# Optimization experiments

Hardware: AMD Instinct MI355X
Metric: run time of the kernel (lower is better)

The kernel has to match this reference:

```python
import jax, jax.numpy as jnp
import numpy as np

NUM_RELATIONS = 8
N_NODES = 50000
N_EDGES = 640000
D_IN = 128
D_HID = 128
N_CLASSES = 16


def rgcn_layer(x, edge_index, edge_type, edge_weight, W):
    # Faithful to ExtendedRGCNConv.forward: per-relation propagate with
    # message = (edge_weight * x_j) @ W[rel]  (== edge_weight * (x_j @ W[rel]))
    # aggregated by scatter-MEAN (PyG RGCNConv default aggr), summed over relations.
    # No root weight / bias (the override skips them).
    src, dst = edge_index[0], edge_index[1]
    num_nodes = x.shape[0]
    out = jnp.zeros((num_nodes, W.shape[2]), dtype=x.dtype)
    for r in range(W.shape[0]):
        sel = edge_type == r
        w = jnp.where(sel, edge_weight, jnp.zeros((), x.dtype))  # [E]
        h = x @ W[r]                                             # [N, out]
        msg = h[src] * w[:, None]                                # [E, out]
        s = jax.ops.segment_sum(msg, dst, num_segments=num_nodes)
        cnt = jax.ops.segment_sum(sel.astype(x.dtype), dst, num_segments=num_nodes)
        out = out + s / jnp.maximum(cnt, 1.0)[:, None]
    return out


def setup_inputs() -> dict:
    key = jax.random.key(0)
    k1, k2, k3, k4, k5, k6 = jax.random.split(key, 6)
    x = jax.random.normal(k1, (N_NODES, D_IN), dtype=jnp.float32)
    edge_index = jax.random.randint(k2, (2, N_EDGES), 0, N_NODES, dtype=jnp.int64)
    edge_type = jax.random.randint(k3, (N_EDGES,), 0, NUM_RELATIONS, dtype=jnp.int64)
    edge_attr = jax.random.uniform(k4, (N_EDGES,), dtype=jnp.float32)
    # Xavier-uniform-ish relation weight banks
    b1 = (6.0 / (D_IN + D_HID)) ** 0.5
    W1 = jax.random.uniform(k5, (NUM_RELATIONS, D_IN, D_HID), minval=-b1, maxval=b1, dtype=jnp.float32)
    b2 = (6.0 / (D_HID + N_CLASSES)) ** 0.5
    W2 = jax.random.uniform(k6, (NUM_RELATIONS, D_HID, N_CLASSES), minval=-b2, maxval=b2, dtype=jnp.float32)
    return {"x": x, "edge_index": edge_index, "edge_type": edge_type, "edge_attr": edge_attr, "W1": W1, "W2": W2}


def reference(x, edge_index, edge_type, edge_attr, W1, W2):
    h = rgcn_layer(x, edge_index, edge_type, edge_attr, W1)
    h = jax.nn.relu(h)
    h = rgcn_layer(h, edge_index, edge_type, edge_attr, W2)
    return jax.nn.log_softmax(h, axis=1)
```

## Files before the change

### kernel.cpp

```cpp
#include <hip/hip_runtime.h>
#include <hip/hip_bf16.h>
#include <math.h>

#define NN 50000
#define EE 640000
#define DD 128
#define NREL 8
#define NCLS 16
#define NBUCK (NREL * NN)
#define SCAN_NB ((NBUCK + 255) / 256)
#define NBIN 64
#define RECCAP 40

typedef __attribute__((ext_vector_type(8))) short short8;
typedef __attribute__((ext_vector_type(4))) float f32x4;

__device__ __forceinline__ float bflo(unsigned u) { return __uint_as_float(u << 16); }
__device__ __forceinline__ float bfhi(unsigned u) { return __uint_as_float(u & 0xffff0000u); }
__device__ __forceinline__ float bf2f(ushort u) { return __uint_as_float(((unsigned)u) << 16); }
__device__ __forceinline__ ushort f2b(float f) {
  unsigned u = __float_as_uint(f);
  u += 0x7fff + ((u >> 16) & 1);
  return (ushort)(u >> 16);
}


__global__ __launch_bounds__(256) void count_kernel(const int* __restrict__ ei,
                                                    const int* __restrict__ et,
                                                    int* __restrict__ cnt) {
  int t = blockIdx.x * 256 + threadIdx.x;
  if (t < EE) {
    int key = ei[EE + t] * NREL + et[t];
    atomicAdd(&cnt[key], 1);
  }
}

__global__ __launch_bounds__(256) void scan1_kernel(const int* __restrict__ cnt,
                                                    int* __restrict__ off,
                                                    int* __restrict__ bsum) {
  __shared__ int s[256];
  const int tid = threadIdx.x;
  const int i = blockIdx.x * 256 + tid;
  int v = (i < NBUCK) ? cnt[i] : 0;
  s[tid] = v;
  __syncthreads();
#pragma unroll
  for (int o = 1; o < 256; o <<= 1) {
    int t2 = (tid >= o) ? s[tid - o] : 0;
    __syncthreads();
    s[tid] += t2;
    __syncthreads();
  }
  if (i < NBUCK) off[i] = s[tid] - v;
  if (tid == 255) bsum[blockIdx.x] = s[255];
}

__global__ __launch_bounds__(256) void scan2_kernel(const int* __restrict__ bsum,
                                                    int* __restrict__ bpre) {
  __shared__ int s[256];
  __shared__ int carry;
  const int tid = threadIdx.x;
  if (tid == 0) carry = 0;
  __syncthreads();
  const int chunks = (SCAN_NB + 255) / 256;
  for (int c = 0; c < chunks; c++) {
    int idx = c * 256 + tid;
    int v = (idx < SCAN_NB) ? bsum[idx] : 0;
    s[tid] = v;
    __syncthreads();
#pragma unroll
    for (int o = 1; o < 256; o <<= 1) {
      int t2 = (tid >= o) ? s[tid - o] : 0;
      __syncthreads();
      s[tid] += t2;
      __syncthreads();
    }
    if (idx < SCAN_NB) bpre[idx] = carry + s[tid] - v;
    __syncthreads();
    if (tid == 255) carry += s[255];
    __syncthreads();
  }
}

__global__ __launch_bounds__(256) void scan3_kernel(int* __restrict__ off,
                                                    const int* __restrict__ bpre,
                                                    int* __restrict__ cursor,
                                                    int* __restrict__ hist) {
  int i = blockIdx.x * 256 + threadIdx.x;
  if (i < NBUCK) {
    int o = off[i] + bpre[i >> 8];
    off[i] = o;
    cursor[i] = o;
  }
  if (i < NBIN) hist[i] = 0;
  if (i == 0) off[NBUCK] = EE;
}

__global__ __launch_bounds__(256) void bucket_kernel(const int* __restrict__ ei,
                                                     const int* __restrict__ et,
                                                     const float* __restrict__ ew,
                                                     const int* __restrict__ cnt,
                                                     int* __restrict__ cursor,
                                                     uint2* __restrict__ rec) {
  int e = blockIdx.x * 256 + threadIdx.x;
  if (e >= EE) return;
  int r = et[e];
  int key = ei[EE + e] * NREL + r;
  float scale = ew[e] / fmaxf((float)cnt[key], 1.0f);
  int pos = atomicAdd(&cursor[key], 1);
  rec[pos] = make_uint2((unsigned)ei[e] | ((unsigned)r << 16), __float_as_uint(scale));
}


__global__ __launch_bounds__(256) void vhist_kernel(const int* __restrict__ off,
                                                    int* __restrict__ hist) {
  __shared__ int lh[NBIN];
  const int tid = threadIdx.x;
  if (tid < NBIN) lh[tid] = 0;
  __syncthreads();
  int v = blockIdx.x * 256 + tid;
  if (v < NN) {
    int deg = off[v * NREL + NREL] - off[v * NREL];
    atomicAdd(&lh[min(deg, NBIN - 1)], 1);
  }
  __syncthreads();
  if (tid < NBIN && lh[tid] > 0) atomicAdd(&hist[tid], lh[tid]);
}

__global__ __launch_bounds__(256) void scan64_kernel(const int* __restrict__ hist,
                                                     int* __restrict__ binCur) {
  __shared__ int s[NBIN];
  const int tid = threadIdx.x;
  if (tid < NBIN) s[tid] = hist[tid];
  __syncthreads();
#pragma unroll
  for (int o = 1; o < NBIN; o <<= 1) {
    int t2 = (tid < NBIN && tid >= o) ? s[tid - o] : 0;
    __syncthreads();
    if (tid < NBIN) s[tid] += t2;
    __syncthreads();
  }
  if (tid < NBIN) binCur[tid] = s[tid] - hist[tid];
}

__global__ __launch_bounds__(256) void vqbuild_kernel(const int* __restrict__ off,
                                                      int* __restrict__ binCur,
                                                      int* __restrict__ vqueue) {
  __shared__ int lh[NBIN];
  __shared__ int lbase[NBIN];
  const int tid = threadIdx.x;
  const int v = blockIdx.x * 256 + tid;
  int bin = -1, lpos = 0;
  if (tid < NBIN) lh[tid] = 0;
  __syncthreads();
  if (v < NN) {
    int deg = off[v * NREL + NREL] - off[v * NREL];
    bin = min(deg, NBIN - 1);
    lpos = atomicAdd(&lh[bin], 1);
  }
  __syncthreads();
  if (tid < NBIN && lh[tid] > 0) lbase[tid] = atomicAdd(&binCur[tid], lh[tid]);
  __syncthreads();
  if (bin >= 0) vqueue[lbase[bin] + lpos] = v;
}

#define XQ (NN * DD / 4)
__global__ __launch_bounds__(256) void pack_kernel(const float* __restrict__ x,
                                                   const float* __restrict__ W1,
                                                   const float* __restrict__ W2,
                                                   ushort* __restrict__ xb,
                                                   ushort* __restrict__ W1Tc,
                                                   ushort* __restrict__ W2T) {
  int t = blockIdx.x * 256 + threadIdx.x;
  if (t < XQ) {
    float4 v = *(const float4*)&x[(size_t)t * 4];
    *(ushort4*)&xb[(size_t)t * 4] = make_ushort4(f2b(v.x), f2b(v.y), f2b(v.z), f2b(v.w));
  } else if (t < XQ + NREL * DD * DD) {
    int t2 = t - XQ;
    int n = t2 >> 10, r = (t2 >> 7) & 7, k = t2 & 127;
    W1Tc[t2] = f2b(W1[r * 16384 + k * 128 + n]);
  } else if (t < XQ + NREL * DD * DD + DD * DD) {
    int t2 = t - XQ - NREL * DD * DD;
    int j = t2 >> 7, k = t2 & 127;
    W2T[t2] = f2b(W2[(j >> 4) * (DD * NCLS) + k * NCLS + (j & 15)]);
  }
}

__global__ __launch_bounds__(512) void fused1_kernel(const int* __restrict__ off,
                                                     const uint2* __restrict__ rec,
                                                     const ushort* __restrict__ xb,
                                                     const ushort* __restrict__ W1Tc,
                                                     const ushort* __restrict__ W2T,
                                                     const int* __restrict__ vqueue,
                                                     ushort* __restrict__ H2) {
  __shared__ ushort AsU[64 * 136];
  __shared__ uint2 recL[64 * RECCAP];
  __shared__ int vids[64];
  const int tid = threadIdx.x;
  const int m0 = blockIdx.x * 64;
  const int wave = tid >> 6, lane = tid & 63;
  const int lm = lane & 15, lkb = (lane >> 4) * 8;
  const int gn = tid >> 3;
  const int gj = tid & 7;
  const int gc = gj * 16;
  const int qi = m0 + gn;
  const int v = (qi < NN) ? vqueue[qi] : -1;
  if (gj == 0) vids[gn] = v;

  int offv[9];
  if (v >= 0) {
    int4 o0 = *(const int4*)&off[v * 8];
    int4 o1 = *(const int4*)&off[v * 8 + 4];
    offv[0] = o0.x; offv[1] = o0.y; offv[2] = o0.z; offv[3] = o0.w;
    offv[4] = o1.x; offv[5] = o1.y; offv[6] = o1.z; offv[7] = o1.w;
    offv[8] = off[v * 8 + 8];
  } else {
#pragma unroll
    for (int i = 0; i < 9; i++) offv[i] = 0;
  }
  const int b0 = offv[0];
  const int rbase = gn * RECCAP;
  {
    int dcap = min(offv[8] - b0, RECCAP);
    for (int i = gj; i < dcap; i += 8) recL[rbase + i] = rec[b0 + i];
  }

#define GETREC(qdst, ii)                                        \
  do {                                                          \
    int _ri = (ii) - b0;                                        \
    if (_ri < RECCAP) qdst = recL[rbase + _ri];                 \
    else qdst = rec[(ii)];                                      \
  } while (0)

  f32x4 acc[4];
#pragma unroll
  for (int m = 0; m < 4; m++) acc[m] = (f32x4){0.f, 0.f, 0.f, 0.f};

#pragma unroll
  for (int r = 0; r < NREL; r++) {
    __syncthreads();
    float g[16];
#pragma unroll
    for (int j = 0; j < 16; j++) g[j] = 0.f;
    {
      int s = offv[r], e = offv[r + 1];
      int i = s;
      for (; i + 2 <= e; i += 2) {
        uint2 q0, q1;
        GETREC(q0, i);
        GETREC(q1, i + 1);
        float sc0 = __uint_as_float(q0.y), sc1 = __uint_as_float(q1.y);
        const ushort* xr0 = &xb[(size_t)(q0.x & 0xffff) * DD + gc];
        const ushort* xr1 = &xb[(size_t)(q1.x & 0xffff) * DD + gc];
        uint4 h0[2], h1[2];
#pragma unroll
        for (int jj = 0; jj < 2; jj++) h0[jj] = *(const uint4*)&xr0[jj * 8];
#pragma unroll
        for (int jj = 0; jj < 2; jj++) h1[jj] = *(const uint4*)&xr1[jj * 8];
#pragma unroll
        for (int jj = 0; jj < 2; jj++) {
          float* gg = &g[jj * 8];
          gg[0] = fmaf(sc0, bflo(h0[jj].x), gg[0]);
          gg[1] = fmaf(sc0, bfhi(h0[jj].x), gg[1]);
          gg[2] = fmaf(sc0, bflo(h0[jj].y), gg[2]);
          gg[3] = fmaf(sc0, bfhi(h0[jj].y), gg[3]);
          gg[4] = fmaf(sc0, bflo(h0[jj].z), gg[4]);
          gg[5] = fmaf(sc0, bfhi(h0[jj].z), gg[5]);
          gg[6] = fmaf(sc0, bflo(h0[jj].w), gg[6]);
          gg[7] = fmaf(sc0, bfhi(h0[jj].w), gg[7]);
          gg[0] = fmaf(sc1, bflo(h1[jj].x), gg[0]);
          gg[1] = fmaf(sc1, bfhi(h1[jj].x), gg[1]);
          gg[2] = fmaf(sc1, bflo(h1[jj].y), gg[2]);
          gg[3] = fmaf(sc1, bfhi(h1[jj].y), gg[3]);
          gg[4] = fmaf(sc1, bflo(h1[jj].z), gg[4]);
          gg[5] = fmaf(sc1, bfhi(h1[jj].z), gg[5]);
          gg[6] = fmaf(sc1, bflo(h1[jj].w), gg[6]);
          gg[7] = fmaf(sc1, bfhi(h1[jj].w), gg[7]);
        }
      }
      if (i < e) {
        uint2 q;
        GETREC(q, i);
        float sc = __uint_as_float(q.y);
        const ushort* xr = &xb[(size_t)(q.x & 0xffff) * DD + gc];
#pragma unroll
        for (int jj = 0; jj < 2; jj++) {
          uint4 h = *(const uint4*)&xr[jj * 8];
          float* gg = &g[jj * 8];
          gg[0] = fmaf(sc, bflo(h.x), gg[0]);
          gg[1] = fmaf(sc, bfhi(h.x), gg[1]);
          gg[2] = fmaf(sc, bflo(h.y), gg[2]);
          gg[3] = fmaf(sc, bfhi(h.y), gg[3]);
          gg[4] = fmaf(sc, bflo(h.z), gg[4]);
          gg[5] = fmaf(sc, bfhi(h.z), gg[5]);
          gg[6] = fmaf(sc, bflo(h.w), gg[6]);
          gg[7] = fmaf(sc, bfhi(h.w), gg[7]);
        }
      }
    }
#pragma unroll
    for (int jj = 0; jj < 2; jj++) {
      uint4 u;
      u.x = (unsigned)f2b(g[jj * 8 + 0]) | ((unsigned)f2b(g[jj * 8 + 1]) << 16);
      u.y = (unsigned)f2b(g[jj * 8 + 2]) | ((unsigned)f2b(g[jj * 8 + 3]) << 16);
      u.z = (unsigned)f2b(g[jj * 8 + 4]) | ((unsigned)f2b(g[jj * 8 + 5]) << 16);
      u.w = (unsigned)f2b(g[jj * 8 + 6]) | ((unsigned)f2b(g[jj * 8 + 7]) << 16);
      *(uint4*)&AsU[gn * 136 + gc + jj * 8] = u;
    }
    __syncthreads();
#pragma unroll
    for (int k0 = 0; k0 < 128; k0 += 32) {
      short8 b = *(const short8*)&W1Tc[(size_t)(wave * 16 + lm) * 1024 + r * 128 + k0 + lkb];
      short8 a[4];
#pragma unroll
      for (int m = 0; m < 4; m++)
        a[m] = *(const short8*)&AsU[(m * 16 + lm) * 136 + k0 + lkb];
#pragma unroll
      for (int m = 0; m < 4; m++)
        acc[m] = __builtin_amdgcn_mfma_f32_16x16x32_bf16(a[m], b, acc[m], 0, 0, 0);
    }
  }
#undef GETREC

  __syncthreads();
  const int rquad = (lane >> 4) * 4;
#pragma unroll
  for (int m = 0; m < 4; m++)
#pragma unroll
    for (int i = 0; i < 4; i++)
      AsU[(m * 16 + rquad + i) * 136 + wave * 16 + lm] = f2b(fmaxf(acc[m][i], 0.f));
  __syncthreads();

  f32x4 acc2[4];
#pragma unroll
  for (int m = 0; m < 4; m++) acc2[m] = (f32x4){0.f, 0.f, 0.f, 0.f};
#pragma unroll
  for (int k0 = 0; k0 < 128; k0 += 32) {
    short8 b = *(const short8*)&W2T[(size_t)(wave * 16 + lm) * DD + k0 + lkb];
    short8 a[4];
#pragma unroll
    for (int m = 0; m < 4; m++)
      a[m] = *(const short8*)&AsU[(m * 16 + lm) * 136 + k0 + lkb];
#pragma unroll
    for (int m = 0; m < 4; m++)
      acc2[m] = __builtin_amdgcn_mfma_f32_16x16x32_bf16(a[m], b, acc2[m], 0, 0, 0);
  }
  __syncthreads();
#pragma unroll
  for (int m = 0; m < 4; m++)
#pragma unroll
    for (int i = 0; i < 4; i++)
      AsU[(m * 16 + rquad + i) * 136 + wave * 16 + lm] = f2b(acc2[m][i]);
  __syncthreads();
#pragma unroll
  for (int i = 0; i < 2; i++) {
    int seg = tid + i * 512;
    int row = seg >> 4, c8 = (seg & 15) * 8;
    int gr = vids[row];
    if (gr >= 0) *(uint4*)&H2[(size_t)gr * DD + c8] = *(const uint4*)&AsU[row * 136 + c8];
  }
}

__global__ __launch_bounds__(256) void gather2_kernel(const int* __restrict__ off,
                                                      const uint2* __restrict__ rec,
                                                      const ushort* __restrict__ H2,
                                                      const int* __restrict__ vqueue,
                                                      float* __restrict__ out) {
  __shared__ uint2 recL[16 * RECCAP];
  const int tid = threadIdx.x;
  const int g = tid >> 4, c = tid & 15;
  const int qi = blockIdx.x * 16 + g;
  int v = 0, s = 0, e = 0;
  if (qi < NN) {
    v = vqueue[qi];
    s = off[v * NREL];
    e = off[v * NREL + NREL];
  }
  const int rbase = g * RECCAP;
  {
    int dcap = min(e - s, RECCAP);
    for (int i = c; i < dcap; i += 16) recL[rbase + i] = rec[s + i];
  }
  __syncthreads();

#define GETREC2(qdst, ii)                                       \
  do {                                                          \
    int _ri = (ii) - s;                                         \
    if (_ri < RECCAP) qdst = recL[rbase + _ri];                 \
    else qdst = rec[(ii)];                                      \
  } while (0)

  float acc = 0.f;
  if (qi < NN) {
    int j = s;
    for (; j + 2 <= e; j += 2) {
      uint2 q0, q1;
      GETREC2(q0, j);
      GETREC2(q1, j + 1);
      ushort h0 = H2[(size_t)(q0.x & 0xffff) * DD + (q0.x >> 16) * NCLS + c];
      ushort h1 = H2[(size_t)(q1.x & 0xffff) * DD + (q1.x >> 16) * NCLS + c];
      acc = fmaf(__uint_as_float(q0.y), bf2f(h0), acc);
      acc = fmaf(__uint_as_float(q1.y), bf2f(h1), acc);
    }
    if (j < e) {
      uint2 q;
      GETREC2(q, j);
      acc = fmaf(__uint_as_float(q.y),
                 bf2f(H2[(size_t)(q.x & 0xffff) * DD + (q.x >> 16) * NCLS + c]), acc);
    }
  }
#undef GETREC2
  float m = acc;
#pragma unroll
  for (int mask = 8; mask >= 1; mask >>= 1) m = fmaxf(m, __shfl_xor(m, mask, 16));
  float ex = expf(acc - m);
#pragma unroll
  for (int mask = 8; mask >= 1; mask >>= 1) ex += __shfl_xor(ex, mask, 16);
  if (qi < NN) out[(size_t)v * NCLS + c] = acc - m - logf(ex);
}

extern "C" void kernel_launch(void* const* d_in, const int* in_sizes, int n_in,
                              void* d_out, int out_size, void* d_ws, size_t ws_size,
                              hipStream_t stream) {
  const float* x  = (const float*)d_in[0];
  const int*   ei = (const int*)d_in[1];
  const int*   et = (const int*)d_in[2];
  const float* ew = (const float*)d_in[3];
  const float* W1 = (const float*)d_in[4];
  const float* W2 = (const float*)d_in[5];
  float* out = (float*)d_out;
  float* ws = (float*)d_ws;

  int*    cnt    = (int*)ws;
  int*    off    = (int*)(ws + 400000);
  int*    bsum   = (int*)(ws + 800004);
  int*    bpre   = (int*)(ws + 801568);
  int*    cursor = (int*)(ws + 803132);
  int*    hist   = (int*)(ws + 1203132);
  int*    binCur = (int*)(ws + 1203196);
  int*    vqueue = (int*)(ws + 1203260);
  uint2*  rec    = (uint2*)(ws + 1253260);
  ushort* xb     = (ushort*)(ws + 2533260);
  ushort* W1Tc   = (ushort*)(ws + 5733260);
  ushort* W2T    = (ushort*)(ws + 5798796);
  ushort* H2     = (ushort*)(ws + 5806988);

  hipMemsetAsync(cnt, 0, (size_t)NBUCK * sizeof(int), stream);

  count_kernel<<<(EE + 255) / 256, 256, 0, stream>>>(ei, et, cnt);
  scan1_kernel<<<SCAN_NB, 256, 0, stream>>>(cnt, off, bsum);
  scan2_kernel<<<1, 256, 0, stream>>>(bsum, bpre);
  scan3_kernel<<<SCAN_NB, 256, 0, stream>>>(off, bpre, cursor, hist);
  bucket_kernel<<<(EE + 255) / 256, 256, 0, stream>>>(ei, et, ew, cnt, cursor, rec);

  vhist_kernel<<<(NN + 255) / 256, 256, 0, stream>>>(off, hist);
  scan64_kernel<<<1, 256, 0, stream>>>(hist, binCur);
  vqbuild_kernel<<<(NN + 255) / 256, 256, 0, stream>>>(off, binCur, vqueue);

  const int packN = XQ + NREL * DD * DD + DD * DD;
  pack_kernel<<<(packN + 255) / 256, 256, 0, stream>>>(x, W1, W2, xb, W1Tc, W2T);

  fused1_kernel<<<(NN + 63) / 64, 512, 0, stream>>>(off, rec, xb, W1Tc, W2T, vqueue, H2);
  gather2_kernel<<<(NN + 15) / 16, 256, 0, stream>>>(off, rec, H2, vqueue, out);
}
```

Measured before the change: 268.4 us.

## Aggregate all relations into one wide tile and run a single K=1024 GEMM

The fused layer-1 kernel now gathers each node's neighbors in one pass over all relations. It accumulates per-relation sums into a 32x1024 shared tile, flushing whenever the relation id in the record changes. It then runs one MFMA GEMM with K=1024 against the concatenated W1 instead of eight per-relation gather/GEMM rounds with barriers in between. Tiles shrink to 32 nodes with 16 threads per node and 8 columns each, which removes per-relation syncs but uses more shared memory and fewer rows per MFMA wave.

```diff
diff --git a/kernel.cpp b/kernel.cpp
--- a/kernel.cpp
+++ b/kernel.cpp
@@ -11,6 +11,7 @@
 #define SCAN_NB ((NBUCK + 255) / 256)
 #define NBIN 64
 #define RECCAP 40
+#define TNODES 32
 
 typedef __attribute__((ext_vector_type(8))) short short8;
 typedef __attribute__((ext_vector_type(4))) float f32x4;
@@ -193,171 +194,151 @@
                                                      const ushort* __restrict__ W2T,
                                                      const int* __restrict__ vqueue,
                                                      ushort* __restrict__ H2) {
-  __shared__ ushort AsU[64 * 136];
-  __shared__ uint2 recL[64 * RECCAP];
-  __shared__ int vids[64];
-  const int tid = threadIdx.x;
-  const int m0 = blockIdx.x * 64;
+  __shared__ ushort At[TNODES * 1032];
+  __shared__ uint2 recL[TNODES * RECCAP];
+  __shared__ int vids[TNODES];
+  const int tid = threadIdx.x;
   const int wave = tid >> 6, lane = tid & 63;
   const int lm = lane & 15, lkb = (lane >> 4) * 8;
-  const int gn = tid >> 3;
-  const int gj = tid & 7;
-  const int gc = gj * 16;
-  const int qi = m0 + gn;
+  const int gn = tid >> 4;
+  const int gj = tid & 15;
+  const int gc = gj * 8;
+  const int qi = blockIdx.x * TNODES + gn;
   const int v = (qi < NN) ? vqueue[qi] : -1;
   if (gj == 0) vids[gn] = v;
 
-  int offv[9];
+  int s = 0, e = 0;
   if (v >= 0) {
-    int4 o0 = *(const int4*)&off[v * 8];
-    int4 o1 = *(const int4*)&off[v * 8 + 4];
-    offv[0] = o0.x; offv[1] = o0.y; offv[2] = o0.z; offv[3] = o0.w;
-    offv[4] = o1.x; offv[5] = o1.y; offv[6] = o1.z; offv[7] = o1.w;
-    offv[8] = off[v * 8 + 8];
-  } else {
-#pragma unroll
-    for (int i = 0; i < 9; i++) offv[i] = 0;
-  }
-  const int b0 = offv[0];
+    s = off[v * 8];
+    e = off[v * 8 + 8];
+  }
+
+  {
+    const int zr = tid >> 4, zc = (tid & 15) * 64;
+#pragma unroll
+    for (int j = 0; j < 8; j++)
+      *(uint4*)&At[zr * 1032 + zc + j * 8] = make_uint4(0u, 0u, 0u, 0u);
+  }
   const int rbase = gn * RECCAP;
   {
-    int dcap = min(offv[8] - b0, RECCAP);
-    for (int i = gj; i < dcap; i += 8) recL[rbase + i] = rec[b0 + i];
-  }
-
-#define GETREC(qdst, ii)                                        \
+    int dcap = min(e - s, RECCAP);
+    for (int i = gj; i < dcap; i += 16) recL[rbase + i] = rec[s + i];
+  }
+  __syncthreads();
+
+#define GETR(q, ii)                                             \
   do {                                                          \
-    int _ri = (ii) - b0;                                        \
-    if (_ri < RECCAP) qdst = recL[rbase + _ri];                 \
-    else qdst = rec[(ii)];                                      \
+    int _ri = (ii) - s;                                         \
+    q = (_ri < RECCAP) ? recL[rbase + _ri] : rec[(ii)];         \
   } while (0)
-
-  f32x4 acc[4];
-#pragma unroll
-  for (int m = 0; m < 4; m++) acc[m] = (f32x4){0.f, 0.f, 0.f, 0.f};
-
-#pragma unroll
-  for (int r = 0; r < NREL; r++) {
-    __syncthreads();
-    float g[16];
-#pragma unroll
-    for (int j = 0; j < 16; j++) g[j] = 0.f;
-    {
-      int s = offv[r], e = offv[r + 1];
-      int i = s;
-      for (; i + 2 <= e; i += 2) {
-        uint2 q0, q1;
-        GETREC(q0, i);
-        GETREC(q1, i + 1);
-        float sc0 = __uint_as_float(q0.y), sc1 = __uint_as_float(q1.y);
-        const ushort* xr0 = &xb[(size_t)(q0.x & 0xffff) * DD + gc];
-        const ushort* xr1 = &xb[(size_t)(q1.x & 0xffff) * DD + gc];
-        uint4 h0[2], h1[2];
-#pragma unroll
-        for (int jj = 0; jj < 2; jj++) h0[jj] = *(const uint4*)&xr0[jj * 8];
-#pragma unroll
-        for (int jj = 0; jj < 2; jj++) h1[jj] = *(const uint4*)&xr1[jj * 8];
-#pragma unroll
-        for (int jj = 0; jj < 2; jj++) {
-          float* gg = &g[jj * 8];
-          gg[0] = fmaf(sc0, bflo(h0[jj].x), gg[0]);
-          gg[1] = fmaf(sc0, bfhi(h0[jj].x), gg[1]);
-          gg[2] = fmaf(sc0, bflo(h0[jj].y), gg[2]);
-          gg[3] = fmaf(sc0, bfhi(h0[jj].y), gg[3]);
-          gg[4] = fmaf(sc0, bflo(h0[jj].z), gg[4]);
-          gg[5] = fmaf(sc0, bfhi(h0[jj].z), gg[5]);
-          gg[6] = fmaf(sc0, bflo(h0[jj].w), gg[6]);
-          gg[7] = fmaf(sc0, bfhi(h0[jj].w), gg[7]);
-          gg[0] = fmaf(sc1, bflo(h1[jj].x), gg[0]);
-          gg[1] = fmaf(sc1, bfhi(h1[jj].x), gg[1]);
-          gg[2] = fmaf(sc1, bflo(h1[jj].y), gg[2]);
-          gg[3] = fmaf(sc1, bfhi(h1[jj].y), gg[3]);
-          gg[4] = fmaf(sc1, bflo(h1[jj].z), gg[4]);
-          gg[5] = fmaf(sc1, bfhi(h1[jj].z), gg[5]);
-          gg[6] = fmaf(sc1, bflo(h1[jj].w), gg[6]);
-          gg[7] = fmaf(sc1, bfhi(h1[jj].w), gg[7]);
-        }
-      }
-      if (i < e) {
-        uint2 q;
-        GETREC(q, i);
-        float sc = __uint_as_float(q.y);
-        const ushort* xr = &xb[(size_t)(q.x & 0xffff) * DD + gc];
-#pragma unroll
-        for (int jj = 0; jj < 2; jj++) {
-          uint4 h = *(const uint4*)&xr[jj * 8];
-          float* gg = &g[jj * 8];
-          gg[0] = fmaf(sc, bflo(h.x), gg[0]);
-          gg[1] = fmaf(sc, bfhi(h.x), gg[1]);
-          gg[2] = fmaf(sc, bflo(h.y), gg[2]);
-          gg[3] = fmaf(sc, bfhi(h.y), gg[3]);
-          gg[4] = fmaf(sc, bflo(h.z), gg[4]);
-          gg[5] = fmaf(sc, bfhi(h.z), gg[5]);
-          gg[6] = fmaf(sc, bflo(h.w), gg[6]);
-          gg[7] = fmaf(sc, bfhi(h.w), gg[7]);
-        }
-      }
+#define LOADE(ii, hv, scv, rv)                                  \
+  do {                                                          \
+    uint2 _q;                                                   \
+    GETR(_q, (ii));                                             \
+    scv = __uint_as_float(_q.y);                                \
+    rv = (int)(_q.x >> 16);                                     \
+    hv = *(const uint4*)&xb[(size_t)(_q.x & 0xffff) * DD + gc]; \
+  } while (0)
+#define FLUSH()                                                   \
+  do {                                                            \
+    uint4 _u;                                                     \
+    _u.x = (unsigned)f2b(g[0]) | ((unsigned)f2b(g[1]) << 16);     \
+    _u.y = (unsigned)f2b(g[2]) | ((unsigned)f2b(g[3]) << 16);     \
+    _u.z = (unsigned)f2b(g[4]) | ((unsigned)f2b(g[5]) << 16);     \
+    _u.w = (unsigned)f2b(g[6]) | ((unsigned)f2b(g[7]) << 16);     \
+    *(uint4*)&At[gn * 1032 + cur * 128 + gc] = _u;                \
+  } while (0)
+#define PROC(hv, scv, rv)                                         \
+  do {                                                            \
+    if (rv != cur) {                                              \
+      if (cur >= 0) FLUSH();                                      \
+      cur = rv;                                                   \
+      g[0] = g[1] = g[2] = g[3] = g[4] = g[5] = g[6] = g[7] = 0.f;\
+    }                                                             \
+    g[0] = fmaf(scv, bflo(hv.x), g[0]);                           \
+    g[1] = fmaf(scv, bfhi(hv.x), g[1]);                           \
+    g[2] = fmaf(scv, bflo(hv.y), g[2]);                           \
+    g[3] = fmaf(scv, bfhi(hv.y), g[3]);                           \
+    g[4] = fmaf(scv, bflo(hv.z), g[4]);                           \
+    g[5] = fmaf(scv, bfhi(hv.z), g[5]);                           \
+    g[6] = fmaf(scv, bflo(hv.w), g[6]);                           \
+    g[7] = fmaf(scv, bfhi(hv.w), g[7]);                           \
+  } while (0)
+
+  {
+    float g[8];
+    g[0] = g[1] = g[2] = g[3] = g[4] = g[5] = g[6] = g[7] = 0.f;
+    int cur = -1;
+    int i = s;
+    for (; i + 4 <= e; i += 4) {
+      uint4 h0, h1, h2, h3;
+      float s0, s1, s2, s3;
+      int r0, r1, r2, r3;
+      LOADE(i, h0, s0, r0);
+      LOADE(i + 1, h1, s1, r1);
+      LOADE(i + 2, h2, s2, r2);
+      LOADE(i + 3, h3, s3, r3);
+      PROC(h0, s0, r0);
+      PROC(h1, s1, r1);
+      PROC(h2, s2, r2);
+      PROC(h3, s3, r3);
     }
-#pragma unroll
-    for (int jj = 0; jj < 2; jj++) {
-      uint4 u;
-      u.x = (unsigned)f2b(g[jj * 8 + 0]) | ((unsigned)f2b(g[jj * 8 + 1]) << 16);
-      u.y = (unsigned)f2b(g[jj * 8 + 2]) | ((unsigned)f2b(g[jj * 8 + 3]) << 16);
-      u.z = (unsigned)f2b(g[jj * 8 + 4]) | ((unsigned)f2b(g[jj * 8 + 5]) << 16);
-      u.w = (unsigned)f2b(g[jj * 8 + 6]) | ((unsigned)f2b(g[jj * 8 + 7]) << 16);
-      *(uint4*)&AsU[gn * 136 + gc + jj * 8] = u;
+    for (; i < e; i++) {
+      uint4 h;
+      float sc;
+      int rl;
+      LOADE(i, h, sc, rl);
+      PROC(h, sc, rl);
     }
-    __syncthreads();
-#pragma unroll
-    for (int k0 = 0; k0 < 128; k0 += 32) {
-      short8 b = *(const short8*)&W1Tc[(size_t)(wave * 16 + lm) * 1024 + r * 128 + k0 + lkb];
-      short8 a[4];
-#pragma unroll
-      for (int m = 0; m < 4; m++)
-        a[m] = *(const short8*)&AsU[(m * 16 + lm) * 136 + k0 + lkb];
-#pragma unroll
-      for (int m = 0; m < 4; m++)
-        acc[m] = __builtin_amdgcn_mfma_f32_16x16x32_bf16(a[m], b, acc[m], 0, 0, 0);
-    }
-  }
-#undef GETREC
-
-  __syncthreads();
+    if (cur >= 0) FLUSH();
+  }
+#undef PROC
+#undef FLUSH
+#undef LOADE
+#undef GETR
+  __syncthreads();
+
+  f32x4 a0 = (f32x4){0.f, 0.f, 0.f, 0.f};
+  f32x4 a1 = (f32x4){0.f, 0.f, 0.f, 0.f};
+#pragma unroll 8
+  for (int kk = 0; kk < 1024; kk += 32) {
+    short8 b = *(const short8*)&W1Tc[(size_t)(wave * 16 + lm) * 1024 + kk + lkb];
+    short8 x0 = *(const short8*)&At[lm * 1032 + kk + lkb];
+    short8 x1 = *(const short8*)&At[(16 + lm) * 1032 + kk + lkb];
+    a0 = __builtin_amdgcn_mfma_f32_16x16x32_bf16(x0, b, a0, 0, 0, 0);
+    a1 = __builtin_amdgcn_mfma_f32_16x16x32_bf16(x1, b, a1, 0, 0, 0);
+  }
+  __syncthreads();
+
   const int rquad = (lane >> 4) * 4;
 #pragma unroll
-  for (int m = 0; m < 4; m++)
-#pragma unroll
-    for (int i = 0; i < 4; i++)
-      AsU[(m * 16 + rquad + i) * 136 + wave * 16 + lm] = f2b(fmaxf(acc[m][i], 0.f));
-  __syncthreads();
-
-  f32x4 acc2[4];
-#pragma unroll
-  for (int m = 0; m < 4; m++) acc2[m] = (f32x4){0.f, 0.f, 0.f, 0.f};
+  for (int i2 = 0; i2 < 4; i2++) {
+    At[(rquad + i2) * 136 + wave * 16 + lm] = f2b(fmaxf(a0[i2], 0.f));
+    At[(16 + rquad + i2) * 136 + wave * 16 + lm] = f2b(fmaxf(a1[i2], 0.f));
+  }
+  __syncthreads();
+
+  f32x4 c0 = (f32x4){0.f, 0.f, 0.f, 0.f};
+  f32x4 c1 = (f32x4){0.f, 0.f, 0.f, 0.f};
 #pragma unroll
   for (int k0 = 0; k0 < 128; k0 += 32) {
     short8 b = *(const short8*)&W2T[(size_t)(wave * 16 + lm) * DD + k0 + lkb];
-    short8 a[4];
-#pragma unroll
-    for (int m = 0; m < 4; m++)
-      a[m] = *(const short8*)&AsU[(m * 16 + lm) * 136 + k0 + lkb];
-#pragma unroll
-    for (int m = 0; m < 4; m++)
-      acc2[m] = __builtin_amdgcn_mfma_f32_16x16x32_bf16(a[m], b, acc2[m], 0, 0, 0);
-  }
-  __syncthreads();
-#pragma unroll
-  for (int m = 0; m < 4; m++)
-#pragma unroll
-    for (int i = 0; i < 4; i++)
-      AsU[(m * 16 + rquad + i) * 136 + wave * 16 + lm] = f2b(acc2[m][i]);
-  __syncthreads();
-#pragma unroll
-  for (int i = 0; i < 2; i++) {
-    int seg = tid + i * 512;
-    int row = seg >> 4, c8 = (seg & 15) * 8;
+    short8 x0 = *(const short8*)&At[lm * 136 + k0 + lkb];
+    short8 x1 = *(const short8*)&At[(16 + lm) * 136 + k0 + lkb];
+    c0 = __builtin_amdgcn_mfma_f32_16x16x32_bf16(x0, b, c0, 0, 0, 0);
+    c1 = __builtin_amdgcn_mfma_f32_16x16x32_bf16(x1, b, c1, 0, 0, 0);
+  }
+  __syncthreads();
+#pragma unroll
+  for (int i2 = 0; i2 < 4; i2++) {
+    At[(rquad + i2) * 136 + wave * 16 + lm] = f2b(c0[i2]);
+    At[(16 + rquad + i2) * 136 + wave * 16 + lm] = f2b(c1[i2]);
+  }
+  __syncthreads();
+  {
+    int row = tid >> 4, c8 = (tid & 15) * 8;
     int gr = vids[row];
-    if (gr >= 0) *(uint4*)&H2[(size_t)gr * DD + c8] = *(const uint4*)&AsU[row * 136 + c8];
+    if (gr >= 0) *(uint4*)&H2[(size_t)gr * DD + c8] = *(const uint4*)&At[row * 136 + c8];
   }
 }
 
@@ -460,6 +441,6 @@
   const int packN = XQ + NREL * DD * DD + DD * DD;
   pack_kernel<<<(packN + 255) / 256, 256, 0, stream>>>(x, W1, W2, xb, W1Tc, W2T);
 
-  fused1_kernel<<<(NN + 63) / 64, 512, 0, stream>>>(off, rec, xb, W1Tc, W2T, vqueue, H2);
+  fused1_kernel<<<(NN + TNODES - 1) / TNODES, 512, 0, stream>>>(off, rec, xb, W1Tc, W2T, vqueue, H2);
   gather2_kernel<<<(NN + 15) / 16, 256, 0, stream>>>(off, rec, H2, vqueue, out);
 }
```

Result: slower. 280.9 us (+4.7%).

## Drop degree-sorted vertex queue, fuse pack into count, use wave-shuffle scan

Applied to the files above, without the earlier changes.

Removes the degree histogram, bin scan and vertex-queue build kernels, so the fused layer-1 kernel and the layer-2 gather now process vertices in natural order. Merges the bf16 pack of x and weights into the edge-count kernel and rewrites the block-sum scan as a single-wave shuffle scan. The layer-2 gather now uses two lanes per class and combines them with a shuffle. The aim is fewer launches and less serial preprocessing, at the cost of the load balancing the degree sort gave.

```diff
diff --git a/kernel.cpp b/kernel.cpp
--- a/kernel.cpp
+++ b/kernel.cpp
@@ -9,7 +9,6 @@
 #define NCLS 16
 #define NBUCK (NREL * NN)
 #define SCAN_NB ((NBUCK + 255) / 256)
-#define NBIN 64
 #define RECCAP 40
 
 typedef __attribute__((ext_vector_type(8))) short short8;
@@ -24,14 +23,33 @@
   return (ushort)(u >> 16);
 }
 
-
-__global__ __launch_bounds__(256) void count_kernel(const int* __restrict__ ei,
-                                                    const int* __restrict__ et,
-                                                    int* __restrict__ cnt) {
+#define XQ (NN * DD / 4)
+#define PACKN (XQ + NREL * DD * DD + DD * DD)
+__global__ __launch_bounds__(256) void countpack_kernel(const int* __restrict__ ei,
+                                                        const int* __restrict__ et,
+                                                        const float* __restrict__ x,
+                                                        const float* __restrict__ W1,
+                                                        const float* __restrict__ W2,
+                                                        int* __restrict__ cnt,
+                                                        ushort* __restrict__ xb,
+                                                        ushort* __restrict__ W1Tc,
+                                                        ushort* __restrict__ W2T) {
   int t = blockIdx.x * 256 + threadIdx.x;
   if (t < EE) {
     int key = ei[EE + t] * NREL + et[t];
     atomicAdd(&cnt[key], 1);
+  }
+  if (t < XQ) {
+    float4 v = *(const float4*)&x[(size_t)t * 4];
+    *(ushort4*)&xb[(size_t)t * 4] = make_ushort4(f2b(v.x), f2b(v.y), f2b(v.z), f2b(v.w));
+  } else if (t < XQ + NREL * DD * DD) {
+    int t2 = t - XQ;
+    int n = t2 >> 10, r = (t2 >> 7) & 7, k = t2 & 127;
+    W1Tc[t2] = f2b(W1[r * 16384 + k * 128 + n]);
+  } else if (t < PACKN) {
+    int t2 = t - XQ - NREL * DD * DD;
+    int j = t2 >> 7, k = t2 & 127;
+    W2T[t2] = f2b(W2[(j >> 4) * (DD * NCLS) + k * NCLS + (j & 15)]);
   }
 }
 
@@ -55,44 +73,33 @@
   if (tid == 255) bsum[blockIdx.x] = s[255];
 }
 
-__global__ __launch_bounds__(256) void scan2_kernel(const int* __restrict__ bsum,
-                                                    int* __restrict__ bpre) {
-  __shared__ int s[256];
-  __shared__ int carry;
-  const int tid = threadIdx.x;
-  if (tid == 0) carry = 0;
-  __syncthreads();
-  const int chunks = (SCAN_NB + 255) / 256;
-  for (int c = 0; c < chunks; c++) {
-    int idx = c * 256 + tid;
-    int v = (idx < SCAN_NB) ? bsum[idx] : 0;
-    s[tid] = v;
-    __syncthreads();
-#pragma unroll
-    for (int o = 1; o < 256; o <<= 1) {
-      int t2 = (tid >= o) ? s[tid - o] : 0;
-      __syncthreads();
-      s[tid] += t2;
-      __syncthreads();
-    }
-    if (idx < SCAN_NB) bpre[idx] = carry + s[tid] - v;
-    __syncthreads();
-    if (tid == 255) carry += s[255];
-    __syncthreads();
+__global__ __launch_bounds__(64) void scan2_kernel(const int* __restrict__ bsum,
+                                                   int* __restrict__ bpre) {
+  const int lane = threadIdx.x;
+  int carry = 0;
+  for (int base = 0; base < SCAN_NB; base += 64) {
+    int idx = base + lane;
+    int own = (idx < SCAN_NB) ? bsum[idx] : 0;
+    int v = own;
+#pragma unroll
+    for (int o = 1; o < 64; o <<= 1) {
+      int t = __shfl_up(v, o, 64);
+      if (lane >= o) v += t;
+    }
+    if (idx < SCAN_NB) bpre[idx] = carry + v - own;
+    carry += __shfl(v, 63, 64);
   }
 }
 
 __global__ __launch_bounds__(256) void scan3_kernel(int* __restrict__ off,
                                                     const int* __restrict__ bpre,
-                                                    int* __restrict__ cursor,
-                                                    int* __restrict__ hist) {
+                                                    int* __restrict__ cursor) {
   int i = blockIdx.x * 256 + threadIdx.x;
   if (i < NBUCK) {
     int o = off[i] + bpre[i >> 8];
     off[i] = o;
     cursor[i] = o;
   }
-  if (i < NBIN) hist[i] = 0;
   if (i == 0) off[NBUCK] = EE;
 }
 
@@ -111,91 +118,14 @@
   rec[pos] = make_uint2((unsigned)ei[e] | ((unsigned)r << 16), __float_as_uint(scale));
 }
 
-
-__global__ __launch_bounds__(256) void vhist_kernel(const int* __restrict__ off,
-                                                    int* __restrict__ hist) {
-  __shared__ int lh[NBIN];
-  const int tid = threadIdx.x;
-  if (tid < NBIN) lh[tid] = 0;
-  __syncthreads();
-  int v = blockIdx.x * 256 + tid;
-  if (v < NN) {
-    int deg = off[v * NREL + NREL] - off[v * NREL];
-    atomicAdd(&lh[min(deg, NBIN - 1)], 1);
-  }
-  __syncthreads();
-  if (tid < NBIN && lh[tid] > 0) atomicAdd(&hist[tid], lh[tid]);
-}
-
-__global__ __launch_bounds__(256) void scan64_kernel(const int* __restrict__ hist,
-                                                     int* __restrict__ binCur) {
-  __shared__ int s[NBIN];
-  const int tid = threadIdx.x;
-  if (tid < NBIN) s[tid] = hist[tid];
-  __syncthreads();
-#pragma unroll
-  for (int o = 1; o < NBIN; o <<= 1) {
-    int t2 = (tid < NBIN && tid >= o) ? s[tid - o] : 0;
-    __syncthreads();
-    if (tid < NBIN) s[tid] += t2;
-    __syncthreads();
-  }
-  if (tid < NBIN) binCur[tid] = s[tid] - hist[tid];
-}
-
-__global__ __launch_bounds__(256) void vqbuild_kernel(const int* __restrict__ off,
-                                                      int* __restrict__ binCur,
-                                                      int* __restrict__ vqueue) {
-  __shared__ int lh[NBIN];
-  __shared__ int lbase[NBIN];
-  const int tid = threadIdx.x;
-  const int v = blockIdx.x * 256 + tid;
-  int bin = -1, lpos = 0;
-  if (tid < NBIN) lh[tid] = 0;
-  __syncthreads();
-  if (v < NN) {
-    int deg = off[v * NREL + NREL] - off[v * NREL];
-    bin = min(deg, NBIN - 1);
-    lpos = atomicAdd(&lh[bin], 1);
-  }
-  __syncthreads();
-  if (tid < NBIN && lh[tid] > 0) lbase[tid] = atomicAdd(&binCur[tid], lh[tid]);
-  __syncthreads();
-  if (bin >= 0) vqueue[lbase[bin] + lpos] = v;
-}
-
-#define XQ (NN * DD / 4)
-__global__ __launch_bounds__(256) void pack_kernel(const float* __restrict__ x,
-                                                   const float* __restrict__ W1,
-                                                   const float* __restrict__ W2,
-                                                   ushort* __restrict__ xb,
-                                                   ushort* __restrict__ W1Tc,
-                                                   ushort* __restrict__ W2T) {
-  int t = blockIdx.x * 256 + threadIdx.x;
-  if (t < XQ) {
-    float4 v = *(const float4*)&x[(size_t)t * 4];
-    *(ushort4*)&xb[(size_t)t * 4] = make_ushort4(f2b(v.x), f2b(v.y), f2b(v.z), f2b(v.w));
-  } else if (t < XQ + NREL * DD * DD) {
-    int t2 = t - XQ;
-    int n = t2 >> 10, r = (t2 >> 7) & 7, k = t2 & 127;
-    W1Tc[t2] = f2b(W1[r * 16384 + k * 128 + n]);
-  } else if (t < XQ + NREL * DD * DD + DD * DD) {
-    int t2 = t - XQ - NREL * DD * DD;
-    int j = t2 >> 7, k = t2 & 127;
-    W2T[t2] = f2b(W2[(j >> 4) * (DD * NCLS) + k * NCLS + (j & 15)]);
-  }
-}
-
 __global__ __launch_bounds__(512) void fused1_kernel(const int* __restrict__ off,
                                                      const uint2* __restrict__ rec,
                                                      const ushort* __restrict__ xb,
                                                      const ushort* __restrict__ W1Tc,
                                                      const ushort* __restrict__ W2T,
-                                                     const int* __restrict__ vqueue,
                                                      ushort* __restrict__ H2) {
   __shared__ ushort AsU[64 * 136];
   __shared__ uint2 recL[64 * RECCAP];
-  __shared__ int vids[64];
   const int tid = threadIdx.x;
   const int m0 = blockIdx.x * 64;
   const int wave = tid >> 6, lane = tid & 63;
@@ -203,12 +133,10 @@
   const int gn = tid >> 3;
   const int gj = tid & 7;
   const int gc = gj * 16;
-  const int qi = m0 + gn;
-  const int v = (qi < NN) ? vqueue[qi] : -1;
-  if (gj == 0) vids[gn] = v;
+  const int v = m0 + gn;
 
   int offv[9];
-  if (v >= 0) {
+  if (v < NN) {
     int4 o0 = *(const int4*)&off[v * 8];
     int4 o1 = *(const int4*)&off[v * 8 + 4];
     offv[0] = o0.x; offv[1] = o0.y; offv[2] = o0.z; offv[3] = o0.w;
@@ -356,30 +284,31 @@
   for (int i = 0; i < 2; i++) {
     int seg = tid + i * 512;
     int row = seg >> 4, c8 = (seg & 15) * 8;
-    int gr = vids[row];
-    if (gr >= 0) *(uint4*)&H2[(size_t)gr * DD + c8] = *(const uint4*)&AsU[row * 136 + c8];
+    int gr = m0 + row;
+    if (gr < NN) *(uint4*)&H2[(size_t)gr * DD + c8] = *(const uint4*)&AsU[row * 136 + c8];
   }
 }
 
 __global__ __launch_bounds__(256) void gather2_kernel(const int* __restrict__ off,
                                                       const uint2* __restrict__ rec,
                                                       const ushort* __restrict__ H2,
-                                                      const int* __restrict__ vqueue,
                                                       float* __restrict__ out) {
-  __shared__ uint2 recL[16 * RECCAP];
+  __shared__ uint2 recL[8 * RECCAP];
   const int tid = threadIdx.x;
-  const int g = tid >> 4, c = tid & 15;
-  const int qi = blockIdx.x * 16 + g;
-  int v = 0, s = 0, e = 0;
-  if (qi < NN) {
-    v = vqueue[qi];
+  const int g = tid >> 5;
+  const int sub = tid & 31;
+  const int j = sub >> 4;
+  const int c = sub & 15;
+  const int v = blockIdx.x * 8 + g;
+  int s = 0, e = 0;
+  if (v < NN) {
     s = off[v * NREL];
     e = off[v * NREL + NREL];
   }
   const int rbase = g * RECCAP;
   {
     int dcap = min(e - s, RECCAP);
-    for (int i = c; i < dcap; i += 16) recL[rbase + i] = rec[s + i];
+    for (int i = sub; i < dcap; i += 32) recL[rbase + i] = rec[s + i];
   }
   __syncthreads();
 
@@ -391,32 +320,33 @@
   } while (0)
 
   float acc = 0.f;
-  if (qi < NN) {
-    int j = s;
-    for (; j + 2 <= e; j += 2) {
+  if (v < NN) {
+    int i = s + j;
+    for (; i + 2 < e; i += 4) {
       uint2 q0, q1;
-      GETREC2(q0, j);
-      GETREC2(q1, j + 1);
+      GETREC2(q0, i);
+      GETREC2(q1, i + 2);
       ushort h0 = H2[(size_t)(q0.x & 0xffff) * DD + (q0.x >> 16) * NCLS + c];
       ushort h1 = H2[(size_t)(q1.x & 0xffff) * DD + (q1.x >> 16) * NCLS + c];
       acc = fmaf(__uint_as_float(q0.y), bf2f(h0), acc);
       acc = fmaf(__uint_as_float(q1.y), bf2f(h1), acc);
     }
-    if (j < e) {
+    for (; i < e; i += 2) {
       uint2 q;
-      GETREC2(q, j);
+      GETREC2(q, i);
       acc = fmaf(__uint_as_float(q.y),
                  bf2f(H2[(size_t)(q.x & 0xffff) * DD + (q.x >> 16) * NCLS + c]), acc);
     }
   }
 #undef GETREC2
+  acc += __shfl_xor(acc, 16, 32);
   float m = acc;
 #pragma unroll
   for (int mask = 8; mask >= 1; mask >>= 1) m = fmaxf(m, __shfl_xor(m, mask, 16));
   float ex = expf(acc - m);
 #pragma unroll
   for (int mask = 8; mask >= 1; mask >>= 1) ex += __shfl_xor(ex, mask, 16);
-  if (qi < NN) out[(size_t)v * NCLS + c] = acc - m - logf(ex);
+  if (v < NN && j == 0) out[(size_t)v * NCLS + c] = acc - m - logf(ex);
 }
 
 extern "C" void kernel_launch(void* const* d_in, const int* in_sizes, int n_in,
@@ -436,30 +366,20 @@
   int*    bsum   = (int*)(ws + 800004);
   int*    bpre   = (int*)(ws + 801568);
   int*    cursor = (int*)(ws + 803132);
-  int*    hist   = (int*)(ws + 1203132);
-  int*    binCur = (int*)(ws + 1203196);
-  int*    vqueue = (int*)(ws + 1203260);
-  uint2*  rec    = (uint2*)(ws + 1253260);
-  ushort* xb     = (ushort*)(ws + 2533260);
-  ushort* W1Tc   = (ushort*)(ws + 5733260);
-  ushort* W2T    = (ushort*)(ws + 5798796);
-  ushort* H2     = (ushort*)(ws + 5806988);
+  uint2*  rec    = (uint2*)(ws + 1203132);
+  ushort* xb     = (ushort*)(ws + 2483132);
+  ushort* W1Tc   = (ushort*)(ws + 5683132);
+  ushort* W2T    = (ushort*)(ws + 5748668);
+  ushort* H2     = (ushort*)(ws + 5756860);
 
   hipMemsetAsync(cnt, 0, (size_t)NBUCK * sizeof(int), stream);
 
-  count_kernel<<<(EE + 255) / 256, 256, 0, stream>>>(ei, et, cnt);
+  countpack_kernel<<<(PACKN + 255) / 256, 256, 0, stream>>>(ei, et, x, W1, W2, cnt, xb, W1Tc, W2T);
   scan1_kernel<<<SCAN_NB, 256, 0, stream>>>(cnt, off, bsum);
-  scan2_kernel<<<1, 256, 0, stream>>>(bsum, bpre);
-  scan3_kernel<<<SCAN_NB, 256, 0, stream>>>(off, bpre, cursor, hist);
+  scan2_kernel<<<1, 64, 0, stream>>>(bsum, bpre);
+  scan3_kernel<<<SCAN_NB, 256, 0, stream>>>(off, bpre, cursor);
   bucket_kernel<<<(EE + 255) / 256, 256, 0, stream>>>(ei, et, ew, cnt, cursor, rec);
 
-  vhist_kernel<<<(NN + 255) / 256, 256, 0, stream>>>(off, hist);
-  scan64_kernel<<<1, 256, 0, stream>>>(hist, binCur);
-  vqbuild_kernel<<<(NN + 255) / 256, 256, 0, stream>>>(off, binCur, vqueue);
-
-  const int packN = XQ + NREL * DD * DD + DD * DD;
-  pack_kernel<<<(packN + 255) / 256, 256, 0, stream>>>(x, W1, W2, xb, W1Tc, W2T);
-
-  fused1_kernel<<<(NN + 63) / 64, 512, 0, stream>>>(off, rec, xb, W1Tc, W2T, vqueue, H2);
-  gather2_kernel<<<(NN + 15) / 16, 256, 0, stream>>>(off, rec, H2, vqueue, out);
-}
+  fused1_kernel<<<(NN + 63) / 64, 512, 0, stream>>>(off, rec, xb, W1Tc, W2T, H2);
+  gather2_kernel<<<(NN + 7) / 8, 256, 0, stream>>>(off, rec, H2, out);
+}
```

Result: faster. 257.1 us (-4.2%).
